# Kernel tuning notes

Hardware: AMD Instinct MI355X
Metric: run time of the kernel (lower is better)

The kernel has to match this reference:

```python
import jax, jax.numpy as jnp
import numpy as np

QMIN, QMAX = -128, 127  # int8 range, n_bit = 8


def setup_inputs() -> dict:
    key = jax.random.key(0)
    k1, k2, k3, k4 = jax.random.split(key, 4)
    B, S, IN, OUT = 4, 2048, 4096, 4096
    x = jax.random.normal(k1, (B, S, IN), dtype=jnp.float32)
    weight = jax.random.randint(k2, (OUT, IN), QMIN, QMAX + 1, dtype=jnp.int32).astype(jnp.int8)
    scales = (jax.random.uniform(k3, (OUT,), dtype=jnp.float32) * 0.02 + 1e-3)
    zeros = jax.random.randint(k4, (OUT,), -10, 11, dtype=jnp.int32).astype(jnp.float32)
    return {"x": x, "weight": weight, "scales": scales, "zeros": zeros}


def _per_token_dynamic_quant(x):
    # torchao per_token_dynamic_quant: asymmetric int8 quantize per token
    # (over last dim), then dequantize back to float.
    mn = jnp.minimum(jnp.min(x, axis=-1, keepdims=True), 0.0)
    mx = jnp.maximum(jnp.max(x, axis=-1, keepdims=True), 0.0)
    eps = jnp.finfo(jnp.float32).eps
    scale = jnp.maximum((mx - mn) / (QMAX - QMIN), eps)
    zp = jnp.clip(QMIN - jnp.round(mn / scale), QMIN, QMAX)
    q = jnp.clip(jnp.round(x / scale) + zp, QMIN, QMAX)
    return (q - zp) * scale


def reference(x, weight, scales, zeros):
    x_dq = _per_token_dynamic_quant(x.astype(jnp.float32))
    # per-channel (axis 0 = out_features) weight dequant:
    # w_dq[o, i] = (w_int8[o, i] - zeros[o]) * scales[o]
    w_dq = (weight.astype(jnp.float32) - zeros[:, None]) * scales[:, None]
    # F.linear: x @ w_dq.T -> [B, S, OUT]
    return jnp.einsum('bsi,oi->bso', x_dq, w_dq)
```

## Files before the change

kernel.cpp:

```cpp
#include <hip/hip_runtime.h>
#include <stdint.h>

typedef int   v4i __attribute__((ext_vector_type(4)));
typedef float v4f __attribute__((ext_vector_type(4)));

#define TOK_M 8192
#define DIM_K 4096
#define DIM_N 4096
#define BM 128
#define BN 128
#define BK 64

#define GLOAD_LDS16(gsrc, ldst)                                                        \
  __builtin_amdgcn_global_load_lds((const __attribute__((address_space(1))) void*)(gsrc), \
                                   (__attribute__((address_space(3))) void*)(ldst), 16, 0, 0)

__global__ __launch_bounds__(256) void k_pack_w(const int* __restrict__ w,
                                                int8_t* __restrict__ wq,
                                                float* __restrict__ wsumf) {
    __shared__ int sred[4];
    const int row = blockIdx.x;
    const int tid = threadIdx.x;
    const int4* src = (const int4*)(w + (size_t)row * DIM_K) + tid * 4;
    int sum = 0;
    unsigned packed[4];
#pragma unroll
    for (int c = 0; c < 4; ++c) {
        int4 iv = src[c];
        sum += iv.x + iv.y + iv.z + iv.w;
        packed[c] = (unsigned)(iv.x & 255) | ((unsigned)(iv.y & 255) << 8) |
                    ((unsigned)(iv.z & 255) << 16) | ((unsigned)(iv.w & 255) << 24);
    }
    int4 outv = make_int4((int)packed[0], (int)packed[1], (int)packed[2], (int)packed[3]);
    *((int4*)(wq + (size_t)row * DIM_K) + tid) = outv;
#pragma unroll
    for (int off = 32; off; off >>= 1) sum += __shfl_xor(sum, off);
    if ((tid & 63) == 0) sred[tid >> 6] = sum;
    __syncthreads();
    if (tid == 0) wsumf[row] = (float)(sred[0] + sred[1] + sred[2] + sred[3]);
}

__global__ __launch_bounds__(256) void k_quant(const float* __restrict__ x,
                                               int8_t* __restrict__ q,
                                               float* __restrict__ sA,
                                               float* __restrict__ sB,
                                               float* __restrict__ sC) {
    __shared__ float redf[8];
    __shared__ int   redi[4];
    __shared__ float bcast[2];
    const int tok = blockIdx.x;
    const int tid = threadIdx.x;
    const v4f* xr = (const v4f*)(x + (size_t)tok * DIM_K) + tid * 4;
    v4f v[4];
    float mn = 0.0f, mx = 0.0f;
#pragma unroll
    for (int c = 0; c < 4; ++c) {
        v[c] = xr[c];
#pragma unroll
        for (int j = 0; j < 4; ++j) {
            mn = fminf(mn, v[c][j]);
            mx = fmaxf(mx, v[c][j]);
        }
    }
#pragma unroll
    for (int off = 32; off; off >>= 1) {
        mn = fminf(mn, __shfl_xor(mn, off));
        mx = fmaxf(mx, __shfl_xor(mx, off));
    }
    const int wid = tid >> 6;
    if ((tid & 63) == 0) { redf[wid] = mn; redf[4 + wid] = mx; }
    __syncthreads();
    if (tid == 0) {
        float m0 = fminf(fminf(redf[0], redf[1]), fminf(redf[2], redf[3]));
        float m1 = fmaxf(fmaxf(redf[4], redf[5]), fmaxf(redf[6], redf[7]));
        float scale = fmaxf((m1 - m0) / 255.0f, 1.1920928955078125e-07f);
        float zpf = -128.0f - rintf(m0 / scale);
        zpf = fminf(fmaxf(zpf, -128.0f), 127.0f);
        bcast[0] = scale; bcast[1] = zpf;
    }
    __syncthreads();
    const float scale = bcast[0];
    const float zpf   = bcast[1];
    const float inv   = 1.0f / scale;
    int qs = 0;
    unsigned packed[4];
#pragma unroll
    for (int c = 0; c < 4; ++c) {
        unsigned p = 0;
#pragma unroll
        for (int j = 0; j < 4; ++j) {
            float qf = rintf(v[c][j] * inv) + zpf;
            qf = fminf(fmaxf(qf, -128.0f), 127.0f);
            int qi = (int)qf;
            qs += qi;
            p |= ((unsigned)(qi & 255)) << (8 * j);
        }
        packed[c] = p;
    }
    *((int4*)(q + (size_t)tok * DIM_K) + tid) =
        make_int4((int)packed[0], (int)packed[1], (int)packed[2], (int)packed[3]);
#pragma unroll
    for (int off = 32; off; off >>= 1) qs += __shfl_xor(qs, off);
    if ((tid & 63) == 0) redi[wid] = qs;
    __syncthreads();
    if (tid == 0) {
        int qtot = redi[0] + redi[1] + redi[2] + redi[3];
        float t = (float)qtot - 4096.0f * zpf;
        sA[tok] = scale;
        sB[tok] = scale * zpf;
        sC[tok] = scale * t;
    }
}

__global__ __launch_bounds__(256) void k_gemm(const int8_t* __restrict__ A,
                                              const int8_t* __restrict__ B,
                                              const float* __restrict__ sA,
                                              const float* __restrict__ sB,
                                              const float* __restrict__ sC,
                                              const float* __restrict__ wsumf,
                                              const float* __restrict__ scales,
                                              const float* __restrict__ zeros,
                                              float* __restrict__ out) {
    __shared__ int8_t As[BM * BK];
    __shared__ int8_t Bs[BN * BK];
    const int tid = threadIdx.x;
    const int w = tid >> 6;
    const int l = tid & 63;
    const int m0 = blockIdx.y * BM;
    const int n0 = blockIdx.x * BN;

    const int o0 = (w * 2 + 0) * 1024 + l * 16;
    const int o1 = (w * 2 + 1) * 1024 + l * 16;
    const int8_t* a0 = A + (size_t)(m0 + (o0 >> 6)) * DIM_K + (o0 & 63);
    const int8_t* a1 = A + (size_t)(m0 + (o1 >> 6)) * DIM_K + (o1 & 63);
    const int8_t* b0 = B + (size_t)(n0 + (o0 >> 6)) * DIM_K + (o0 & 63);
    const int8_t* b1 = B + (size_t)(n0 + (o1 >> 6)) * DIM_K + (o1 & 63);

    const int wr = (w >> 1) * 64;
    const int wc = (w & 1) * 64;
    const int lr = l & 15;
    const int lg = (l >> 4) * 16;

    v4i acc[4][4] = {};

    for (int k0 = 0; k0 < DIM_K; k0 += BK) {
        GLOAD_LDS16(a0 + k0, As + o0);
        GLOAD_LDS16(a1 + k0, As + o1);
        GLOAD_LDS16(b0 + k0, Bs + o0);
        GLOAD_LDS16(b1 + k0, Bs + o1);
        __syncthreads();

        v4i af[4], bf[4];
#pragma unroll
        for (int mi = 0; mi < 4; ++mi)
            af[mi] = *(const v4i*)(As + (wr + mi * 16 + lr) * BK + lg);
#pragma unroll
        for (int ni = 0; ni < 4; ++ni)
            bf[ni] = *(const v4i*)(Bs + (wc + ni * 16 + lr) * BK + lg);
#pragma unroll
        for (int mi = 0; mi < 4; ++mi)
#pragma unroll
            for (int ni = 0; ni < 4; ++ni)
                acc[mi][ni] = __builtin_amdgcn_mfma_i32_16x16x64_i8(
                    af[mi], bf[ni], acc[mi][ni], 0, 0, 0);
        __syncthreads();
    }

    const int col_l = l & 15;
    const int rg = (l >> 4) * 4;
    float scl[4], zrs[4], wsm[4];
    int gc[4];
#pragma unroll
    for (int ni = 0; ni < 4; ++ni) {
        gc[ni] = n0 + wc + ni * 16 + col_l;
        scl[ni] = scales[gc[ni]];
        zrs[ni] = zeros[gc[ni]];
        wsm[ni] = wsumf[gc[ni]];
    }
#pragma unroll
    for (int mi = 0; mi < 4; ++mi) {
#pragma unroll
        for (int j = 0; j < 4; ++j) {
            const int gr = m0 + wr + mi * 16 + rg + j;
            const float ra = sA[gr];
            const float rb = sB[gr];
            const float rc = sC[gr];
            float* orow = out + (size_t)gr * DIM_N;
#pragma unroll
            for (int ni = 0; ni < 4; ++ni) {
                float accf = (float)acc[mi][ni][j];
                orow[gc[ni]] = scl[ni] * (ra * accf - rb * wsm[ni] - rc * zrs[ni]);
            }
        }
    }
}

extern "C" void kernel_launch(void* const* d_in, const int* in_sizes, int n_in,
                              void* d_out, int out_size, void* d_ws, size_t ws_size,
                              hipStream_t stream) {
    const float* x      = (const float*)d_in[0];
    const int*   w      = (const int*)d_in[1];
    const float* scales = (const float*)d_in[2];
    const float* zeros  = (const float*)d_in[3];
    float* out = (float*)d_out;

    uint8_t* ws = (uint8_t*)d_ws;
    int8_t* q  = (int8_t*)ws;
    int8_t* wq = (int8_t*)(ws + (size_t)TOK_M * DIM_K);
    float* fbuf = (float*)(ws + (size_t)TOK_M * DIM_K + (size_t)DIM_N * DIM_K);
    float* sA    = fbuf;
    float* sB    = fbuf + TOK_M;
    float* sC    = fbuf + 2 * TOK_M;
    float* wsumf = fbuf + 3 * TOK_M;

    k_pack_w<<<DIM_N, 256, 0, stream>>>(w, wq, wsumf);
    k_quant<<<TOK_M, 256, 0, stream>>>(x, q, sA, sB, sC);
    dim3 grid(DIM_N / BN, TOK_M / BM);
    k_gemm<<<grid, 256, 0, stream>>>(q, wq, sA, sB, sC, wsumf, scales, zeros, out);
}
```

Before: 434.1 us.

## Rewrite int8 GEMM with 256x256 tiles, triple-buffered LDS pipeline and swizzles

```diff
diff --git a/kernel.cpp b/kernel.cpp
--- a/kernel.cpp
+++ b/kernel.cpp
@@ -7,13 +7,10 @@
 #define TOK_M 8192
 #define DIM_K 4096
 #define DIM_N 4096
-#define BM 128
-#define BN 128
-#define BK 64
-
-#define GLOAD_LDS16(gsrc, ldst)                                                        \
-  __builtin_amdgcn_global_load_lds((const __attribute__((address_space(1))) void*)(gsrc), \
-                                   (__attribute__((address_space(3))) void*)(ldst), 16, 0, 0)
+
+#define GL(src, dst)                                                                   \
+  __builtin_amdgcn_global_load_lds((const __attribute__((address_space(1))) void*)(src), \
+                                   (__attribute__((address_space(3))) void*)(dst), 16, 0, 0)
 
 __global__ __launch_bounds__(256) void k_pack_w(const int* __restrict__ w,
                                                 int8_t* __restrict__ wq,
@@ -21,18 +18,17 @@
     __shared__ int sred[4];
     const int row = blockIdx.x;
     const int tid = threadIdx.x;
-    const int4* src = (const int4*)(w + (size_t)row * DIM_K) + tid * 4;
+    const int4* src = (const int4*)(w + (size_t)row * DIM_K);
+    unsigned* dst = (unsigned*)(wq + (size_t)row * DIM_K);
     int sum = 0;
-    unsigned packed[4];
 #pragma unroll
     for (int c = 0; c < 4; ++c) {
-        int4 iv = src[c];
+        int4 iv = src[c * 256 + tid];
         sum += iv.x + iv.y + iv.z + iv.w;
-        packed[c] = (unsigned)(iv.x & 255) | ((unsigned)(iv.y & 255) << 8) |
-                    ((unsigned)(iv.z & 255) << 16) | ((unsigned)(iv.w & 255) << 24);
-    }
-    int4 outv = make_int4((int)packed[0], (int)packed[1], (int)packed[2], (int)packed[3]);
-    *((int4*)(wq + (size_t)row * DIM_K) + tid) = outv;
+        unsigned p = (unsigned)(iv.x & 255) | ((unsigned)(iv.y & 255) << 8) |
+                     ((unsigned)(iv.z & 255) << 16) | ((unsigned)(iv.w & 255) << 24);
+        dst[c * 256 + tid] = p;
+    }
 #pragma unroll
     for (int off = 32; off; off >>= 1) sum += __shfl_xor(sum, off);
     if ((tid & 63) == 0) sred[tid >> 6] = sum;
@@ -50,12 +46,12 @@
     __shared__ float bcast[2];
     const int tok = blockIdx.x;
     const int tid = threadIdx.x;
-    const v4f* xr = (const v4f*)(x + (size_t)tok * DIM_K) + tid * 4;
+    const v4f* xr = (const v4f*)(x + (size_t)tok * DIM_K);
     v4f v[4];
     float mn = 0.0f, mx = 0.0f;
 #pragma unroll
     for (int c = 0; c < 4; ++c) {
-        v[c] = xr[c];
+        v[c] = xr[c * 256 + tid];
 #pragma unroll
         for (int j = 0; j < 4; ++j) {
             mn = fminf(mn, v[c][j]);
@@ -83,7 +79,7 @@
     const float zpf   = bcast[1];
     const float inv   = 1.0f / scale;
     int qs = 0;
-    unsigned packed[4];
+    unsigned* qo = (unsigned*)(q + (size_t)tok * DIM_K);
 #pragma unroll
     for (int c = 0; c < 4; ++c) {
         unsigned p = 0;
@@ -95,102 +91,155 @@
             qs += qi;
             p |= ((unsigned)(qi & 255)) << (8 * j);
         }
-        packed[c] = p;
-    }
-    *((int4*)(q + (size_t)tok * DIM_K) + tid) =
-        make_int4((int)packed[0], (int)packed[1], (int)packed[2], (int)packed[3]);
+        qo[c * 256 + tid] = p;
+    }
 #pragma unroll
     for (int off = 32; off; off >>= 1) qs += __shfl_xor(qs, off);
     if ((tid & 63) == 0) redi[wid] = qs;
     __syncthreads();
     if (tid == 0) {
         int qtot = redi[0] + redi[1] + redi[2] + redi[3];
-        float t = (float)qtot - 4096.0f * zpf;
         sA[tok] = scale;
         sB[tok] = scale * zpf;
-        sC[tok] = scale * t;
-    }
-}
-
-__global__ __launch_bounds__(256) void k_gemm(const int8_t* __restrict__ A,
-                                              const int8_t* __restrict__ B,
-                                              const float* __restrict__ sA,
-                                              const float* __restrict__ sB,
-                                              const float* __restrict__ sC,
-                                              const float* __restrict__ wsumf,
-                                              const float* __restrict__ scales,
-                                              const float* __restrict__ zeros,
-                                              float* __restrict__ out) {
-    __shared__ int8_t As[BM * BK];
-    __shared__ int8_t Bs[BN * BK];
+        sC[tok] = scale * ((float)qtot - 4096.0f * zpf);
+    }
+}
+
+#define MFMA8(mI, afR)                                                                     \
+    acc[mI][0] = __builtin_amdgcn_mfma_i32_16x16x64_i8(afR, bf0, acc[mI][0], 0, 0, 0);     \
+    acc[mI][1] = __builtin_amdgcn_mfma_i32_16x16x64_i8(afR, bf1, acc[mI][1], 0, 0, 0);     \
+    acc[mI][2] = __builtin_amdgcn_mfma_i32_16x16x64_i8(afR, bf2, acc[mI][2], 0, 0, 0);     \
+    acc[mI][3] = __builtin_amdgcn_mfma_i32_16x16x64_i8(afR, bf3, acc[mI][3], 0, 0, 0);
+
+__global__ __launch_bounds__(512, 2) void k_gemm(const int8_t* __restrict__ A,
+                                                 const int8_t* __restrict__ B,
+                                                 const float* __restrict__ sA,
+                                                 const float* __restrict__ sB,
+                                                 const float* __restrict__ sC,
+                                                 const float* __restrict__ wsumf,
+                                                 const float* __restrict__ scales,
+                                                 const float* __restrict__ zeros,
+                                                 float* __restrict__ out) {
+    extern __shared__ int8_t lds[];
     const int tid = threadIdx.x;
-    const int w = tid >> 6;
     const int l = tid & 63;
-    const int m0 = blockIdx.y * BM;
-    const int n0 = blockIdx.x * BN;
-
-    const int o0 = (w * 2 + 0) * 1024 + l * 16;
-    const int o1 = (w * 2 + 1) * 1024 + l * 16;
-    const int8_t* a0 = A + (size_t)(m0 + (o0 >> 6)) * DIM_K + (o0 & 63);
-    const int8_t* a1 = A + (size_t)(m0 + (o1 >> 6)) * DIM_K + (o1 & 63);
-    const int8_t* b0 = B + (size_t)(n0 + (o0 >> 6)) * DIM_K + (o0 & 63);
-    const int8_t* b1 = B + (size_t)(n0 + (o1 >> 6)) * DIM_K + (o1 & 63);
-
-    const int wr = (w >> 1) * 64;
-    const int wc = (w & 1) * 64;
-    const int lr = l & 15;
-    const int lg = (l >> 4) * 16;
-
-    v4i acc[4][4] = {};
-
-    for (int k0 = 0; k0 < DIM_K; k0 += BK) {
-        GLOAD_LDS16(a0 + k0, As + o0);
-        GLOAD_LDS16(a1 + k0, As + o1);
-        GLOAD_LDS16(b0 + k0, Bs + o0);
-        GLOAD_LDS16(b1 + k0, Bs + o1);
-        __syncthreads();
-
-        v4i af[4], bf[4];
-#pragma unroll
-        for (int mi = 0; mi < 4; ++mi)
-            af[mi] = *(const v4i*)(As + (wr + mi * 16 + lr) * BK + lg);
-#pragma unroll
-        for (int ni = 0; ni < 4; ++ni)
-            bf[ni] = *(const v4i*)(Bs + (wc + ni * 16 + lr) * BK + lg);
-#pragma unroll
-        for (int mi = 0; mi < 4; ++mi)
-#pragma unroll
-            for (int ni = 0; ni < 4; ++ni)
-                acc[mi][ni] = __builtin_amdgcn_mfma_i32_16x16x64_i8(
-                    af[mi], bf[ni], acc[mi][ni], 0, 0, 0);
-        __syncthreads();
-    }
-
-    const int col_l = l & 15;
-    const int rg = (l >> 4) * 4;
-    float scl[4], zrs[4], wsm[4];
-    int gc[4];
-#pragma unroll
-    for (int ni = 0; ni < 4; ++ni) {
-        gc[ni] = n0 + wc + ni * 16 + col_l;
-        scl[ni] = scales[gc[ni]];
-        zrs[ni] = zeros[gc[ni]];
-        wsm[ni] = wsumf[gc[ni]];
-    }
-#pragma unroll
-    for (int mi = 0; mi < 4; ++mi) {
+    const int wid = tid >> 6;
+
+    const int bswz = (blockIdx.x & 7) * 64 + (blockIdx.x >> 3);
+    const int tm = (bswz & 31) * 256;
+    const int tn = (bswz >> 5) * 256;
+
+    const int sr  = tid >> 2;
+    const int scg = (tid & 3) ^ ((tid >> 3) & 3);
+    const int8_t* aS0 = A + (size_t)(tm + sr) * DIM_K + scg * 16;
+    const int8_t* aS1 = A + (size_t)(tm + 128 + sr) * DIM_K + scg * 16;
+    const int8_t* bS0 = B + (size_t)(tn + sr) * DIM_K + scg * 16;
+    const int8_t* bS1 = B + (size_t)(tn + 128 + sr) * DIM_K + scg * 16;
+    const int dA0 = tid * 16;
+    const int dA1 = 8192 + tid * 16;
+
+    const int i  = l & 15;
+    const int ch = l >> 4;
+    const int pos = ch ^ ((i >> 1) & 3);
+    const int wm = (wid >> 2) * 128;
+    const int wn = (wid & 3) * 64;
+    const int aOff = (wm + i) * 64 + pos * 16;
+    const int bOff = 16384 + (wn + i) * 64 + pos * 16;
+
+    v4i acc[8][4] = {};
+
+    GL(aS0, lds + dA0);          GL(aS1, lds + dA1);
+    GL(bS0, lds + 16384 + dA0);  GL(bS1, lds + 16384 + dA1);
+    GL(aS0 + 64, lds + 32768 + dA0);          GL(aS1 + 64, lds + 32768 + dA1);
+    GL(bS0 + 64, lds + 32768 + 16384 + dA0);  GL(bS1 + 64, lds + 32768 + 16384 + dA1);
+    asm volatile("s_waitcnt vmcnt(4)" ::: "memory");
+    __builtin_amdgcn_s_barrier();
+
+    int cb = 0, sb = 2;
+    for (int kt = 0; kt < 64; ++kt) {
+        const int koff = kt * 64 + 128;
+        int8_t* Sc = lds + cb * 32768;
+        int8_t* St = lds + sb * 32768;
+        const bool doStage = (kt < 62);
+        v4i bf0, bf1, bf2, bf3;
+
+        if (doStage) GL(aS0 + koff, St + dA0);
+        bf0 = *(const v4i*)(Sc + bOff);
+        bf1 = *(const v4i*)(Sc + bOff + 1024);
+        bf2 = *(const v4i*)(Sc + bOff + 2048);
+        bf3 = *(const v4i*)(Sc + bOff + 3072);
+        {
+            v4i a0 = *(const v4i*)(Sc + aOff);
+            v4i a1 = *(const v4i*)(Sc + aOff + 1024);
+            __builtin_amdgcn_sched_barrier(0);
+            __builtin_amdgcn_s_setprio(1);
+            MFMA8(0, a0) MFMA8(1, a1)
+            __builtin_amdgcn_s_setprio(0);
+            __builtin_amdgcn_sched_barrier(0);
+        }
+        __builtin_amdgcn_s_barrier();
+
+        if (doStage) GL(aS1 + koff, St + dA1);
+        {
+            v4i a2 = *(const v4i*)(Sc + aOff + 2048);
+            v4i a3 = *(const v4i*)(Sc + aOff + 3072);
+            __builtin_amdgcn_sched_barrier(0);
+            __builtin_amdgcn_s_setprio(1);
+            MFMA8(2, a2) MFMA8(3, a3)
+            __builtin_amdgcn_s_setprio(0);
+            __builtin_amdgcn_sched_barrier(0);
+        }
+        __builtin_amdgcn_s_barrier();
+
+        if (doStage) GL(bS0 + koff, St + 16384 + dA0);
+        {
+            v4i a4 = *(const v4i*)(Sc + aOff + 4096);
+            v4i a5 = *(const v4i*)(Sc + aOff + 5120);
+            __builtin_amdgcn_sched_barrier(0);
+            __builtin_amdgcn_s_setprio(1);
+            MFMA8(4, a4) MFMA8(5, a5)
+            __builtin_amdgcn_s_setprio(0);
+            __builtin_amdgcn_sched_barrier(0);
+        }
+        __builtin_amdgcn_s_barrier();
+
+        if (doStage) GL(bS1 + koff, St + 16384 + dA1);
+        {
+            v4i a6 = *(const v4i*)(Sc + aOff + 6144);
+            v4i a7 = *(const v4i*)(Sc + aOff + 7168);
+            __builtin_amdgcn_sched_barrier(0);
+            __builtin_amdgcn_s_setprio(1);
+            MFMA8(6, a6) MFMA8(7, a7)
+            __builtin_amdgcn_s_setprio(0);
+            __builtin_amdgcn_sched_barrier(0);
+        }
+        if (kt < 62) { asm volatile("s_waitcnt vmcnt(4)" ::: "memory"); }
+        else         { asm volatile("s_waitcnt vmcnt(0)" ::: "memory"); }
+        __builtin_amdgcn_s_barrier();
+
+        cb = (cb == 2) ? 0 : cb + 1;
+        sb = (sb == 2) ? 0 : sb + 1;
+    }
+
+    const int gr0 = tm + wm + ch * 4;
+    const int gc0 = tn + wn + i;
+    float scl[4], zr[4], wsm[4];
+#pragma unroll
+    for (int n = 0; n < 4; ++n) {
+        const int gc = gc0 + n * 16;
+        scl[n] = scales[gc]; zr[n] = zeros[gc]; wsm[n] = wsumf[gc];
+    }
+#pragma unroll
+    for (int m = 0; m < 8; ++m) {
 #pragma unroll
         for (int j = 0; j < 4; ++j) {
-            const int gr = m0 + wr + mi * 16 + rg + j;
-            const float ra = sA[gr];
-            const float rb = sB[gr];
-            const float rc = sC[gr];
+            const int gr = gr0 + m * 16 + j;
+            const float ra = sA[gr], rb = sB[gr], rc = sC[gr];
             float* orow = out + (size_t)gr * DIM_N;
 #pragma unroll
-            for (int ni = 0; ni < 4; ++ni) {
-                float accf = (float)acc[mi][ni][j];
-                orow[gc[ni]] = scl[ni] * (ra * accf - rb * wsm[ni] - rc * zrs[ni]);
-            }
+            for (int n = 0; n < 4; ++n)
+                orow[gc0 + n * 16] =
+                    scl[n] * (ra * (float)acc[m][n][j] - rb * wsm[n] - rc * zr[n]);
         }
     }
 }
@@ -215,6 +264,5 @@
 
     k_pack_w<<<DIM_N, 256, 0, stream>>>(w, wq, wsumf);
     k_quant<<<TOK_M, 256, 0, stream>>>(x, q, sA, sB, sC);
-    dim3 grid(DIM_N / BN, TOK_M / BM);
-    k_gemm<<<grid, 256, 0, stream>>>(q, wq, sA, sB, sC, wsumf, scales, zeros, out);
-}
+    k_gemm<<<512, 512, 98304, stream>>>(q, wq, sA, sB, sC, wsumf, scales, zeros, out);
+}
```

After: 416.8 us. -4.0%, faster.
